# Kernel optimization log

Hardware: AMD Instinct MI355X
Metric: run time of the kernel (lower is better)

The kernel has to match this reference:

```python
import jax, jax.numpy as jnp
import numpy as np
from jax import lax

B, T, H = 128, 8192, 96


def setup_inputs() -> dict:
    key = jax.random.key(0)
    ks = jax.random.split(key, 7)
    s = 1.0 / np.sqrt(H)  # PyTorch LSTM init scale
    return {
        "x": jax.random.normal(ks[0], (B, T, 1), dtype=jnp.float32),
        "w_ih": jax.random.uniform(ks[1], (4 * H, 1), jnp.float32, -s, s),
        "w_hh": jax.random.uniform(ks[2], (4 * H, H), jnp.float32, -s, s),
        "b_ih": jax.random.uniform(ks[3], (4 * H,), jnp.float32, -s, s),
        "b_hh": jax.random.uniform(ks[4], (4 * H,), jnp.float32, -s, s),
        "w_out": jax.random.uniform(ks[5], (1, H), jnp.float32, -s, s),
        "b_out": jax.random.uniform(ks[6], (1,), jnp.float32, -s, s),
    }


def reference(x, w_ih, w_hh, b_ih, b_hh, w_out, b_out):
    # x: [B, T, 1]; single-layer batch_first LSTM, zero initial (h, c).
    Bb, Tt, _ = x.shape
    Hh = w_hh.shape[1]
    # Precompute input contribution to all gates: [T, B, 4H]
    xg = jnp.einsum("bti,gi->btg", x, w_ih) + b_ih + b_hh
    xg = jnp.transpose(xg, (1, 0, 2))

    def step(carry, g):
        h, c = carry
        gates = g + h @ w_hh.T  # [B, 4H]
        i, f, gg, o = jnp.split(gates, 4, axis=-1)  # PyTorch order: i, f, g, o
        i = jax.nn.sigmoid(i)
        f = jax.nn.sigmoid(f)
        gg = jnp.tanh(gg)
        o = jax.nn.sigmoid(o)
        c = f * c + i * gg
        h = o * jnp.tanh(c)
        return (h, c), h

    h0 = jnp.zeros((Bb, Hh), x.dtype)
    (_, _), hs = lax.scan(step, (h0, h0), xg)  # hs: [T, B, H]
    hs = jnp.transpose(hs, (1, 0, 2))  # [B, T, H]
    return hs @ w_out.T + b_out  # [B, T, 1]
```

## Files before the change

kernel.cpp:

```cpp
#include <hip/hip_runtime.h>


#define T_LEN 8192
#define H_DIM 96
#define NTHR  320
#define CHUNK 128
#define LOG2E 1.44269504f

typedef float    f32x4 __attribute__((ext_vector_type(4)));
typedef _Float16 half8 __attribute__((ext_vector_type(8)));

#define MFMA16(A, B, C)                                                        \
    __builtin_amdgcn_mfma_f32_16x16x32_f16(__builtin_bit_cast(half8, (A)),     \
                                           __builtin_bit_cast(half8, (B)),     \
                                           (C), 0, 0, 0)

__device__ __forceinline__ float sig2(float s) {
    return __builtin_amdgcn_rcpf(1.0f + __builtin_amdgcn_exp2f(-s));
}
__device__ __forceinline__ float tanh2(float sg) {
    return 1.0f - 2.0f * __builtin_amdgcn_rcpf(1.0f + __builtin_amdgcn_exp2f(sg));
}

__device__ __forceinline__ f32x4 load_afrag(const float* __restrict__ w_hh,
                                            const float* __restrict__ w_out,
                                            int mt, int kt, int m, int quad) {
    half8 f;
    if (mt < 24) {
        const int r = m & 3;
        const float scale = (r == 2) ? 2.0f * LOG2E : LOG2E;
        const int orig = r * 96 + 4 * mt + (m >> 2);
        const float* src = w_hh + orig * H_DIM + kt * 32 + quad * 8;
        #pragma unroll
        for (int jj = 0; jj < 8; ++jj) f[jj] = (_Float16)(scale * src[jj]);
    } else {
        #pragma unroll
        for (int jj = 0; jj < 8; ++jj)
            f[jj] = (m == 0) ? (_Float16)w_out[kt * 32 + quad * 8 + jj]
                             : (_Float16)0.0f;
    }
    return __builtin_bit_cast(f32x4, f);
}

__global__ __launch_bounds__(NTHR, 2) void lstm_mfma16_kernel(
    const float* __restrict__ x,
    const float* __restrict__ w_ih,
    const float* __restrict__ w_hh,
    const float* __restrict__ b_ih,
    const float* __restrict__ b_hh,
    const float* __restrict__ w_out,
    const float* __restrict__ b_out,
    float* __restrict__ y)
{
    const int tid  = threadIdx.x;
    const int wv   = tid >> 6;
    const int lane = tid & 63;
    const int m    = lane & 15;
    const int quad = lane >> 4;
    const int cc   = m & 7;
    const int bsub = m >> 3;

    __shared__ __align__(16) _Float16 h_s[2][2][H_DIM];
    __shared__ __align__(16) float    y_buf[2][2][CHUNK];
    __shared__ __align__(16) float    x_s[2][T_LEN + 8];

    {
        const float* xpair = x + (size_t)(2 * blockIdx.x) * T_LEN;
        for (int i = tid * 4; i < T_LEN; i += NTHR * 4) {
            *reinterpret_cast<f32x4*>(&x_s[0][i]) =
                *reinterpret_cast<const f32x4*>(&xpair[i]);
            *reinterpret_cast<f32x4*>(&x_s[1][i]) =
                *reinterpret_cast<const f32x4*>(&xpair[T_LEN + i]);
        }
    }

    const int mt0 = 6 * wv;
    f32x4 af00 = load_afrag(w_hh, w_out, mt0 + 0, 0, m, quad);
    f32x4 af01 = load_afrag(w_hh, w_out, mt0 + 0, 1, m, quad);
    f32x4 af02 = load_afrag(w_hh, w_out, mt0 + 0, 2, m, quad);
    f32x4 af10 = load_afrag(w_hh, w_out, mt0 + 1, 0, m, quad);
    f32x4 af11 = load_afrag(w_hh, w_out, mt0 + 1, 1, m, quad);
    f32x4 af12 = load_afrag(w_hh, w_out, mt0 + 1, 2, m, quad);
    f32x4 af20 = load_afrag(w_hh, w_out, mt0 + 2, 0, m, quad);
    f32x4 af21 = load_afrag(w_hh, w_out, mt0 + 2, 1, m, quad);
    f32x4 af22 = load_afrag(w_hh, w_out, mt0 + 2, 2, m, quad);
    f32x4 af30 = load_afrag(w_hh, w_out, mt0 + 3, 0, m, quad);
    f32x4 af31 = load_afrag(w_hh, w_out, mt0 + 3, 1, m, quad);
    f32x4 af32 = load_afrag(w_hh, w_out, mt0 + 3, 2, m, quad);
    f32x4 af40 = load_afrag(w_hh, w_out, mt0 + 4, 0, m, quad);
    f32x4 af41 = load_afrag(w_hh, w_out, mt0 + 4, 1, m, quad);
    f32x4 af42 = load_afrag(w_hh, w_out, mt0 + 4, 2, m, quad);
    f32x4 af50 = load_afrag(w_hh, w_out, mt0 + 5, 0, m, quad);
    f32x4 af51 = load_afrag(w_hh, w_out, mt0 + 5, 1, m, quad);
    f32x4 af52 = load_afrag(w_hh, w_out, mt0 + 5, 2, m, quad);
    f32x4 zero4 = {0.f, 0.f, 0.f, 0.f};
    asm volatile("" : "+v"(af00), "+v"(af01), "+v"(af02), "+v"(af10),
                      "+v"(af11), "+v"(af12), "+v"(af20));
    asm volatile("" : "+v"(af21), "+v"(af22), "+v"(af30), "+v"(af31),
                      "+v"(af32), "+v"(af40), "+v"(af41));
    asm volatile("" : "+v"(af42), "+v"(af50), "+v"(af51), "+v"(af52),
                      "+v"(zero4));

    f32x4 woa0 = {0,0,0,0}, woa1 = {0,0,0,0}, wob0 = {0,0,0,0},
          wob1 = {0,0,0,0}, woc0 = {0,0,0,0}, woc1 = {0,0,0,0};
    if (wv == 4) {
        woa0 = *reinterpret_cast<const f32x4*>(&w_out[quad * 8]);
        woa1 = *reinterpret_cast<const f32x4*>(&w_out[quad * 8 + 4]);
        wob0 = *reinterpret_cast<const f32x4*>(&w_out[32 + quad * 8]);
        wob1 = *reinterpret_cast<const f32x4*>(&w_out[32 + quad * 8 + 4]);
        woc0 = *reinterpret_cast<const f32x4*>(&w_out[64 + quad * 8]);
        woc1 = *reinterpret_cast<const f32x4*>(&w_out[64 + quad * 8 + 4]);
    }

    const int sel  = (cc >= 6) ? (cc - 6) : cc;
    const int cell = (wv < 4) ? (24 * wv + 4 * sel + quad) : 0;
    const bool s_b0 = sel & 1;
    const bool s_b1 = (sel >> 1) & 1;
    const bool s_b2 = (sel >> 2) & 1;
    const float bias_i = LOG2E * (b_ih[0 * H_DIM + cell] + b_hh[0 * H_DIM + cell]);
    const float bias_f = LOG2E * (b_ih[1 * H_DIM + cell] + b_hh[1 * H_DIM + cell]);
    const float bias_g = 2.0f * LOG2E * (b_ih[2 * H_DIM + cell] + b_hh[2 * H_DIM + cell]);
    const float bias_o = LOG2E * (b_ih[3 * H_DIM + cell] + b_hh[3 * H_DIM + cell]);
    const float wih_i  = LOG2E * w_ih[0 * H_DIM + cell];
    const float wih_f  = LOG2E * w_ih[1 * H_DIM + cell];
    const float wih_g  = 2.0f * LOG2E * w_ih[2 * H_DIM + cell];
    const float wih_o  = LOG2E * w_ih[3 * H_DIM + cell];
    const float bout   = b_out[0];
    float c = 0.f;
    if (tid < 2 * H_DIM) (&h_s[0][0][0])[tid] = (_Float16)0.0f;
    __syncthreads();

    if (wv < 4) __builtin_amdgcn_s_setprio(1);

    float x_cur_next = x_s[bsub][0];

    #pragma unroll 2
    for (int it = 0; it <= T_LEN + 1; ++it) {
        const int p = it & 1;

        if (wv < 4) {
            if (it < T_LEN) {
                const f32x4 b0 = *reinterpret_cast<const f32x4*>(&h_s[p][bsub][quad * 8]);
                const f32x4 b1 = *reinterpret_cast<const f32x4*>(&h_s[p][bsub][32 + quad * 8]);
                const f32x4 b2 = *reinterpret_cast<const f32x4*>(&h_s[p][bsub][64 + quad * 8]);
                const float x_cur = x_cur_next;
                x_cur_next = x_s[bsub][it + 1];

                f32x4 acc0 = MFMA16(af00, b0, zero4);
                f32x4 acc1 = MFMA16(af10, b0, zero4);
                f32x4 acc2 = MFMA16(af20, b0, zero4);
                f32x4 acc3 = MFMA16(af30, b0, zero4);
                f32x4 acc4 = MFMA16(af40, b0, zero4);
                f32x4 acc5 = MFMA16(af50, b0, zero4);
                acc0 = MFMA16(af01, b1, acc0);
                acc1 = MFMA16(af11, b1, acc1);
                acc2 = MFMA16(af21, b1, acc2);
                acc3 = MFMA16(af31, b1, acc3);
                acc4 = MFMA16(af41, b1, acc4);
                acc5 = MFMA16(af51, b1, acc5);
                acc0 = MFMA16(af02, b2, acc0);
                acc1 = MFMA16(af12, b2, acc1);
                acc2 = MFMA16(af22, b2, acc2);
                acc3 = MFMA16(af32, b2, acc3);
                acc4 = MFMA16(af42, b2, acc4);
                acc5 = MFMA16(af52, b2, acc5);

                const f32x4 t0 = s_b0 ? acc1 : acc0;
                const f32x4 t1 = s_b0 ? acc3 : acc2;
                const f32x4 t2 = s_b0 ? acc5 : acc4;
                const f32x4 g4 = s_b2 ? t2 : (s_b1 ? t1 : t0);

                const float s0 = g4.x + fmaf(x_cur, wih_i, bias_i);
                const float s1 = g4.y + fmaf(x_cur, wih_f, bias_f);
                const float s2 = g4.z + fmaf(x_cur, wih_g, bias_g);
                const float s3 = g4.w + fmaf(x_cur, wih_o, bias_o);
                const float ig = sig2(s0);
                const float fg = sig2(s1);
                const float gg = tanh2(s2);
                const float og = sig2(s3);
                c = fmaf(fg, c, ig * gg);
                const float h = og * tanh2(2.0f * LOG2E * c);
                h_s[p ^ 1][bsub][cell] = (_Float16)h;
            }
        } else {
            if (it <= T_LEN) {
                const f32x4 b0 = *reinterpret_cast<const f32x4*>(&h_s[p][bsub][quad * 8]);
                const f32x4 b1 = *reinterpret_cast<const f32x4*>(&h_s[p][bsub][32 + quad * 8]);
                const f32x4 b2 = *reinterpret_cast<const f32x4*>(&h_s[p][bsub][64 + quad * 8]);
                const half8 hb0 = __builtin_bit_cast(half8, b0);
                const half8 hb1 = __builtin_bit_cast(half8, b1);
                const half8 hb2 = __builtin_bit_cast(half8, b2);
                float a0 = 0.f, a1 = 0.f, a2 = 0.f;
                a0 = fmaf((float)hb0[0], woa0.x, a0);
                a1 = fmaf((float)hb1[0], wob0.x, a1);
                a2 = fmaf((float)hb2[0], woc0.x, a2);
                a0 = fmaf((float)hb0[1], woa0.y, a0);
                a1 = fmaf((float)hb1[1], wob0.y, a1);
                a2 = fmaf((float)hb2[1], woc0.y, a2);
                a0 = fmaf((float)hb0[2], woa0.z, a0);
                a1 = fmaf((float)hb1[2], wob0.z, a1);
                a2 = fmaf((float)hb2[2], woc0.z, a2);
                a0 = fmaf((float)hb0[3], woa0.w, a0);
                a1 = fmaf((float)hb1[3], wob0.w, a1);
                a2 = fmaf((float)hb2[3], woc0.w, a2);
                a0 = fmaf((float)hb0[4], woa1.x, a0);
                a1 = fmaf((float)hb1[4], wob1.x, a1);
                a2 = fmaf((float)hb2[4], woc1.x, a2);
                a0 = fmaf((float)hb0[5], woa1.y, a0);
                a1 = fmaf((float)hb1[5], wob1.y, a1);
                a2 = fmaf((float)hb2[5], woc1.y, a2);
                a0 = fmaf((float)hb0[6], woa1.z, a0);
                a1 = fmaf((float)hb1[6], wob1.z, a1);
                a2 = fmaf((float)hb2[6], woc1.z, a2);
                a0 = fmaf((float)hb0[7], woa1.w, a0);
                a1 = fmaf((float)hb1[7], wob1.w, a1);
                a2 = fmaf((float)hb2[7], woc1.w, a2);
                float acc = a0 + a1 + a2;
                acc += __shfl_xor(acc, 32, 64);
                acc += __shfl_xor(acc, 16, 64);
                if ((lane == 0 || lane == 8) && it > 0)
                    y_buf[bsub][((it - 1) >> 7) & 1][(it - 1) & (CHUNK - 1)] =
                        acc + bout;
            }
            if ((it & (CHUNK - 1)) == 1 && it > 1) {
                const int base = it - 1 - CHUNK;
                const int pb   = (base >> 7) & 1;
                const int bsel = lane >> 5;
                const int li   = lane & 31;
                const f32x4 v =
                    *reinterpret_cast<const f32x4*>(&y_buf[bsel][pb][li * 4]);
                float* yrow = y + (size_t)(2 * blockIdx.x + bsel) * T_LEN;
                *reinterpret_cast<f32x4*>(&yrow[base + li * 4]) = v;
            }
        }
        __syncthreads();
    }
}

extern "C" void kernel_launch(void* const* d_in, const int* in_sizes, int n_in,
                              void* d_out, int out_size, void* d_ws, size_t ws_size,
                              hipStream_t stream) {
    const float* x     = (const float*)d_in[0];
    const float* w_ih  = (const float*)d_in[1];
    const float* w_hh  = (const float*)d_in[2];
    const float* b_ih  = (const float*)d_in[3];
    const float* b_hh  = (const float*)d_in[4];
    const float* w_out = (const float*)d_in[5];
    const float* b_out = (const float*)d_in[6];
    float* y = (float*)d_out;

    const int NBLK = 64;
    lstm_mfma16_kernel<<<dim3(NBLK), dim3(NTHR), 0, stream>>>(
        x, w_ih, w_hh, b_ih, b_hh, w_out, b_out, y);
}
```

Measured before the change: 3.078 ms.

## Fold output projection into recurrent wave and drop dedicated output wave

```diff
diff --git a/kernel.cpp b/kernel.cpp
--- a/kernel.cpp
+++ b/kernel.cpp
@@ -3,7 +3,7 @@
 
 #define T_LEN 8192
 #define H_DIM 96
-#define NTHR  320
+#define NTHR  256
 #define CHUNK 128
 #define LOG2E 1.44269504f
 
@@ -23,26 +23,18 @@
 }
 
 __device__ __forceinline__ f32x4 load_afrag(const float* __restrict__ w_hh,
-                                            const float* __restrict__ w_out,
                                             int mt, int kt, int m, int quad) {
     half8 f;
-    if (mt < 24) {
-        const int r = m & 3;
-        const float scale = (r == 2) ? 2.0f * LOG2E : LOG2E;
-        const int orig = r * 96 + 4 * mt + (m >> 2);
-        const float* src = w_hh + orig * H_DIM + kt * 32 + quad * 8;
-        #pragma unroll
-        for (int jj = 0; jj < 8; ++jj) f[jj] = (_Float16)(scale * src[jj]);
-    } else {
-        #pragma unroll
-        for (int jj = 0; jj < 8; ++jj)
-            f[jj] = (m == 0) ? (_Float16)w_out[kt * 32 + quad * 8 + jj]
-                             : (_Float16)0.0f;
-    }
+    const int r = m & 3;
+    const float scale = (r == 2) ? 2.0f * LOG2E : LOG2E;
+    const int orig = r * 96 + 4 * mt + (m >> 2);
+    const float* src = w_hh + orig * H_DIM + kt * 32 + quad * 8;
+    #pragma unroll
+    for (int jj = 0; jj < 8; ++jj) f[jj] = (_Float16)(scale * src[jj]);
     return __builtin_bit_cast(f32x4, f);
 }
 
-__global__ __launch_bounds__(NTHR, 2) void lstm_mfma16_kernel(
+__global__ __launch_bounds__(NTHR, 2) void lstm_mfma17_kernel(
     const float* __restrict__ x,
     const float* __restrict__ w_ih,
     const float* __restrict__ w_hh,
@@ -75,24 +67,24 @@
     }
 
     const int mt0 = 6 * wv;
-    f32x4 af00 = load_afrag(w_hh, w_out, mt0 + 0, 0, m, quad);
-    f32x4 af01 = load_afrag(w_hh, w_out, mt0 + 0, 1, m, quad);
-    f32x4 af02 = load_afrag(w_hh, w_out, mt0 + 0, 2, m, quad);
-    f32x4 af10 = load_afrag(w_hh, w_out, mt0 + 1, 0, m, quad);
-    f32x4 af11 = load_afrag(w_hh, w_out, mt0 + 1, 1, m, quad);
-    f32x4 af12 = load_afrag(w_hh, w_out, mt0 + 1, 2, m, quad);
-    f32x4 af20 = load_afrag(w_hh, w_out, mt0 + 2, 0, m, quad);
-    f32x4 af21 = load_afrag(w_hh, w_out, mt0 + 2, 1, m, quad);
-    f32x4 af22 = load_afrag(w_hh, w_out, mt0 + 2, 2, m, quad);
-    f32x4 af30 = load_afrag(w_hh, w_out, mt0 + 3, 0, m, quad);
-    f32x4 af31 = load_afrag(w_hh, w_out, mt0 + 3, 1, m, quad);
-    f32x4 af32 = load_afrag(w_hh, w_out, mt0 + 3, 2, m, quad);
-    f32x4 af40 = load_afrag(w_hh, w_out, mt0 + 4, 0, m, quad);
-    f32x4 af41 = load_afrag(w_hh, w_out, mt0 + 4, 1, m, quad);
-    f32x4 af42 = load_afrag(w_hh, w_out, mt0 + 4, 2, m, quad);
-    f32x4 af50 = load_afrag(w_hh, w_out, mt0 + 5, 0, m, quad);
-    f32x4 af51 = load_afrag(w_hh, w_out, mt0 + 5, 1, m, quad);
-    f32x4 af52 = load_afrag(w_hh, w_out, mt0 + 5, 2, m, quad);
+    f32x4 af00 = load_afrag(w_hh, mt0 + 0, 0, m, quad);
+    f32x4 af01 = load_afrag(w_hh, mt0 + 0, 1, m, quad);
+    f32x4 af02 = load_afrag(w_hh, mt0 + 0, 2, m, quad);
+    f32x4 af10 = load_afrag(w_hh, mt0 + 1, 0, m, quad);
+    f32x4 af11 = load_afrag(w_hh, mt0 + 1, 1, m, quad);
+    f32x4 af12 = load_afrag(w_hh, mt0 + 1, 2, m, quad);
+    f32x4 af20 = load_afrag(w_hh, mt0 + 2, 0, m, quad);
+    f32x4 af21 = load_afrag(w_hh, mt0 + 2, 1, m, quad);
+    f32x4 af22 = load_afrag(w_hh, mt0 + 2, 2, m, quad);
+    f32x4 af30 = load_afrag(w_hh, mt0 + 3, 0, m, quad);
+    f32x4 af31 = load_afrag(w_hh, mt0 + 3, 1, m, quad);
+    f32x4 af32 = load_afrag(w_hh, mt0 + 3, 2, m, quad);
+    f32x4 af40 = load_afrag(w_hh, mt0 + 4, 0, m, quad);
+    f32x4 af41 = load_afrag(w_hh, mt0 + 4, 1, m, quad);
+    f32x4 af42 = load_afrag(w_hh, mt0 + 4, 2, m, quad);
+    f32x4 af50 = load_afrag(w_hh, mt0 + 5, 0, m, quad);
+    f32x4 af51 = load_afrag(w_hh, mt0 + 5, 1, m, quad);
+    f32x4 af52 = load_afrag(w_hh, mt0 + 5, 2, m, quad);
     f32x4 zero4 = {0.f, 0.f, 0.f, 0.f};
     asm volatile("" : "+v"(af00), "+v"(af01), "+v"(af02), "+v"(af10),
                       "+v"(af11), "+v"(af12), "+v"(af20));
@@ -103,7 +95,7 @@
 
     f32x4 woa0 = {0,0,0,0}, woa1 = {0,0,0,0}, wob0 = {0,0,0,0},
           wob1 = {0,0,0,0}, woc0 = {0,0,0,0}, woc1 = {0,0,0,0};
-    if (wv == 4) {
+    if (wv == 0) {
         woa0 = *reinterpret_cast<const f32x4*>(&w_out[quad * 8]);
         woa1 = *reinterpret_cast<const f32x4*>(&w_out[quad * 8 + 4]);
         wob0 = *reinterpret_cast<const f32x4*>(&w_out[32 + quad * 8]);
@@ -111,9 +103,11 @@
         woc0 = *reinterpret_cast<const f32x4*>(&w_out[64 + quad * 8]);
         woc1 = *reinterpret_cast<const f32x4*>(&w_out[64 + quad * 8 + 4]);
     }
+    asm volatile("" : "+v"(woa0), "+v"(woa1), "+v"(wob0), "+v"(wob1),
+                      "+v"(woc0), "+v"(woc1));
 
     const int sel  = (cc >= 6) ? (cc - 6) : cc;
-    const int cell = (wv < 4) ? (24 * wv + 4 * sel + quad) : 0;
+    const int cell = 24 * wv + 4 * sel + quad;
     const bool s_b0 = sel & 1;
     const bool s_b1 = (sel >> 1) & 1;
     const bool s_b2 = (sel >> 2) & 1;
@@ -130,109 +124,108 @@
     if (tid < 2 * H_DIM) (&h_s[0][0][0])[tid] = (_Float16)0.0f;
     __syncthreads();
 
-    if (wv < 4) __builtin_amdgcn_s_setprio(1);
-
     float x_cur_next = x_s[bsub][0];
 
     #pragma unroll 2
     for (int it = 0; it <= T_LEN + 1; ++it) {
         const int p = it & 1;
-
-        if (wv < 4) {
-            if (it < T_LEN) {
-                const f32x4 b0 = *reinterpret_cast<const f32x4*>(&h_s[p][bsub][quad * 8]);
-                const f32x4 b1 = *reinterpret_cast<const f32x4*>(&h_s[p][bsub][32 + quad * 8]);
-                const f32x4 b2 = *reinterpret_cast<const f32x4*>(&h_s[p][bsub][64 + quad * 8]);
-                const float x_cur = x_cur_next;
-                x_cur_next = x_s[bsub][it + 1];
-
-                f32x4 acc0 = MFMA16(af00, b0, zero4);
-                f32x4 acc1 = MFMA16(af10, b0, zero4);
-                f32x4 acc2 = MFMA16(af20, b0, zero4);
-                f32x4 acc3 = MFMA16(af30, b0, zero4);
-                f32x4 acc4 = MFMA16(af40, b0, zero4);
-                f32x4 acc5 = MFMA16(af50, b0, zero4);
-                acc0 = MFMA16(af01, b1, acc0);
-                acc1 = MFMA16(af11, b1, acc1);
-                acc2 = MFMA16(af21, b1, acc2);
-                acc3 = MFMA16(af31, b1, acc3);
-                acc4 = MFMA16(af41, b1, acc4);
-                acc5 = MFMA16(af51, b1, acc5);
-                acc0 = MFMA16(af02, b2, acc0);
-                acc1 = MFMA16(af12, b2, acc1);
-                acc2 = MFMA16(af22, b2, acc2);
-                acc3 = MFMA16(af32, b2, acc3);
-                acc4 = MFMA16(af42, b2, acc4);
-                acc5 = MFMA16(af52, b2, acc5);
-
-                const f32x4 t0 = s_b0 ? acc1 : acc0;
-                const f32x4 t1 = s_b0 ? acc3 : acc2;
-                const f32x4 t2 = s_b0 ? acc5 : acc4;
-                const f32x4 g4 = s_b2 ? t2 : (s_b1 ? t1 : t0);
-
-                const float s0 = g4.x + fmaf(x_cur, wih_i, bias_i);
-                const float s1 = g4.y + fmaf(x_cur, wih_f, bias_f);
-                const float s2 = g4.z + fmaf(x_cur, wih_g, bias_g);
-                const float s3 = g4.w + fmaf(x_cur, wih_o, bias_o);
-                const float ig = sig2(s0);
-                const float fg = sig2(s1);
-                const float gg = tanh2(s2);
-                const float og = sig2(s3);
-                c = fmaf(fg, c, ig * gg);
-                const float h = og * tanh2(2.0f * LOG2E * c);
-                h_s[p ^ 1][bsub][cell] = (_Float16)h;
-            }
-        } else {
-            if (it <= T_LEN) {
-                const f32x4 b0 = *reinterpret_cast<const f32x4*>(&h_s[p][bsub][quad * 8]);
-                const f32x4 b1 = *reinterpret_cast<const f32x4*>(&h_s[p][bsub][32 + quad * 8]);
-                const f32x4 b2 = *reinterpret_cast<const f32x4*>(&h_s[p][bsub][64 + quad * 8]);
-                const half8 hb0 = __builtin_bit_cast(half8, b0);
-                const half8 hb1 = __builtin_bit_cast(half8, b1);
-                const half8 hb2 = __builtin_bit_cast(half8, b2);
-                float a0 = 0.f, a1 = 0.f, a2 = 0.f;
-                a0 = fmaf((float)hb0[0], woa0.x, a0);
-                a1 = fmaf((float)hb1[0], wob0.x, a1);
-                a2 = fmaf((float)hb2[0], woc0.x, a2);
-                a0 = fmaf((float)hb0[1], woa0.y, a0);
-                a1 = fmaf((float)hb1[1], wob0.y, a1);
-                a2 = fmaf((float)hb2[1], woc0.y, a2);
-                a0 = fmaf((float)hb0[2], woa0.z, a0);
-                a1 = fmaf((float)hb1[2], wob0.z, a1);
-                a2 = fmaf((float)hb2[2], woc0.z, a2);
-                a0 = fmaf((float)hb0[3], woa0.w, a0);
-                a1 = fmaf((float)hb1[3], wob0.w, a1);
-                a2 = fmaf((float)hb2[3], woc0.w, a2);
-                a0 = fmaf((float)hb0[4], woa1.x, a0);
-                a1 = fmaf((float)hb1[4], wob1.x, a1);
-                a2 = fmaf((float)hb2[4], woc1.x, a2);
-                a0 = fmaf((float)hb0[5], woa1.y, a0);
-                a1 = fmaf((float)hb1[5], wob1.y, a1);
-                a2 = fmaf((float)hb2[5], woc1.y, a2);
-                a0 = fmaf((float)hb0[6], woa1.z, a0);
-                a1 = fmaf((float)hb1[6], wob1.z, a1);
-                a2 = fmaf((float)hb2[6], woc1.z, a2);
-                a0 = fmaf((float)hb0[7], woa1.w, a0);
-                a1 = fmaf((float)hb1[7], wob1.w, a1);
-                a2 = fmaf((float)hb2[7], woc1.w, a2);
-                float acc = a0 + a1 + a2;
-                acc += __shfl_xor(acc, 32, 64);
-                acc += __shfl_xor(acc, 16, 64);
-                if ((lane == 0 || lane == 8) && it > 0)
-                    y_buf[bsub][((it - 1) >> 7) & 1][(it - 1) & (CHUNK - 1)] =
-                        acc + bout;
-            }
-            if ((it & (CHUNK - 1)) == 1 && it > 1) {
-                const int base = it - 1 - CHUNK;
-                const int pb   = (base >> 7) & 1;
-                const int bsel = lane >> 5;
-                const int li   = lane & 31;
-                const f32x4 v =
-                    *reinterpret_cast<const f32x4*>(&y_buf[bsel][pb][li * 4]);
-                float* yrow = y + (size_t)(2 * blockIdx.x + bsel) * T_LEN;
-                *reinterpret_cast<f32x4*>(&yrow[base + li * 4]) = v;
-            }
-        }
+        const bool rd = (it < T_LEN) || (wv == 0 && it == T_LEN);
+
+        f32x4 b0, b1, b2;
+        const float x_cur = x_cur_next;
+        if (rd) {
+            b0 = *reinterpret_cast<const f32x4*>(&h_s[p][bsub][quad * 8]);
+            b1 = *reinterpret_cast<const f32x4*>(&h_s[p][bsub][32 + quad * 8]);
+            b2 = *reinterpret_cast<const f32x4*>(&h_s[p][bsub][64 + quad * 8]);
+            x_cur_next = x_s[bsub][it + 1];
+        }
+
+        if (it < T_LEN) {
+            f32x4 acc0 = MFMA16(af00, b0, zero4);
+            f32x4 acc1 = MFMA16(af10, b0, zero4);
+            f32x4 acc2 = MFMA16(af20, b0, zero4);
+            f32x4 acc3 = MFMA16(af30, b0, zero4);
+            f32x4 acc4 = MFMA16(af40, b0, zero4);
+            f32x4 acc5 = MFMA16(af50, b0, zero4);
+            acc0 = MFMA16(af01, b1, acc0);
+            acc1 = MFMA16(af11, b1, acc1);
+            acc2 = MFMA16(af21, b1, acc2);
+            acc3 = MFMA16(af31, b1, acc3);
+            acc4 = MFMA16(af41, b1, acc4);
+            acc5 = MFMA16(af51, b1, acc5);
+            acc0 = MFMA16(af02, b2, acc0);
+            acc1 = MFMA16(af12, b2, acc1);
+            acc2 = MFMA16(af22, b2, acc2);
+            acc3 = MFMA16(af32, b2, acc3);
+            acc4 = MFMA16(af42, b2, acc4);
+            acc5 = MFMA16(af52, b2, acc5);
+
+            const f32x4 t0 = s_b0 ? acc1 : acc0;
+            const f32x4 t1 = s_b0 ? acc3 : acc2;
+            const f32x4 t2 = s_b0 ? acc5 : acc4;
+            const f32x4 g4 = s_b2 ? t2 : (s_b1 ? t1 : t0);
+
+            const float s0 = g4.x + fmaf(x_cur, wih_i, bias_i);
+            const float s1 = g4.y + fmaf(x_cur, wih_f, bias_f);
+            const float s2 = g4.z + fmaf(x_cur, wih_g, bias_g);
+            const float s3 = g4.w + fmaf(x_cur, wih_o, bias_o);
+            const float ig = sig2(s0);
+            const float fg = sig2(s1);
+            const float gg = tanh2(s2);
+            const float og = sig2(s3);
+            c = fmaf(fg, c, ig * gg);
+            const float h = og * tanh2(2.0f * LOG2E * c);
+            h_s[p ^ 1][bsub][cell] = (_Float16)h;
+        }
+
+        if (wv == 0 && rd && it > 0) {
+            const half8 hb0 = __builtin_bit_cast(half8, b0);
+            const half8 hb1 = __builtin_bit_cast(half8, b1);
+            const half8 hb2 = __builtin_bit_cast(half8, b2);
+            float a0 = 0.f, a1 = 0.f, a2 = 0.f;
+            a0 = fmaf((float)hb0[0], woa0.x, a0);
+            a1 = fmaf((float)hb1[0], wob0.x, a1);
+            a2 = fmaf((float)hb2[0], woc0.x, a2);
+            a0 = fmaf((float)hb0[1], woa0.y, a0);
+            a1 = fmaf((float)hb1[1], wob0.y, a1);
+            a2 = fmaf((float)hb2[1], woc0.y, a2);
+            a0 = fmaf((float)hb0[2], woa0.z, a0);
+            a1 = fmaf((float)hb1[2], wob0.z, a1);
+            a2 = fmaf((float)hb2[2], woc0.z, a2);
+            a0 = fmaf((float)hb0[3], woa0.w, a0);
+            a1 = fmaf((float)hb1[3], wob0.w, a1);
+            a2 = fmaf((float)hb2[3], woc0.w, a2);
+            a0 = fmaf((float)hb0[4], woa1.x, a0);
+            a1 = fmaf((float)hb1[4], wob1.x, a1);
+            a2 = fmaf((float)hb2[4], woc1.x, a2);
+            a0 = fmaf((float)hb0[5], woa1.y, a0);
+            a1 = fmaf((float)hb1[5], wob1.y, a1);
+            a2 = fmaf((float)hb2[5], woc1.y, a2);
+            a0 = fmaf((float)hb0[6], woa1.z, a0);
+            a1 = fmaf((float)hb1[6], wob1.z, a1);
+            a2 = fmaf((float)hb2[6], woc1.z, a2);
+            a0 = fmaf((float)hb0[7], woa1.w, a0);
+            a1 = fmaf((float)hb1[7], wob1.w, a1);
+            a2 = fmaf((float)hb2[7], woc1.w, a2);
+            float acc = a0 + a1 + a2;
+            acc += __shfl_xor(acc, 32, 64);
+            acc += __shfl_xor(acc, 16, 64);
+            if (lane == 0 || lane == 8)
+                y_buf[bsub][((it - 1) >> 7) & 1][(it - 1) & (CHUNK - 1)] =
+                    acc + bout;
+        }
+
+        if (wv == 1 && (it & (CHUNK - 1)) == 1 && it > 1) {
+            const int base = it - 1 - CHUNK;
+            const int pb   = (base >> 7) & 1;
+            const int bsel = lane >> 5;
+            const int li   = lane & 31;
+            const f32x4 v =
+                *reinterpret_cast<const f32x4*>(&y_buf[bsel][pb][li * 4]);
+            float* yrow = y + (size_t)(2 * blockIdx.x + bsel) * T_LEN;
+            *reinterpret_cast<f32x4*>(&yrow[base + li * 4]) = v;
+        }
+
         __syncthreads();
     }
 }
@@ -250,6 +243,6 @@
     float* y = (float*)d_out;
 
     const int NBLK = 64;
-    lstm_mfma16_kernel<<<dim3(NBLK), dim3(NTHR), 0, stream>>>(
+    lstm_mfma17_kernel<<<dim3(NBLK), dim3(NTHR), 0, stream>>>(
         x, w_ih, w_hh, b_ih, b_hh, w_out, b_out, y);
 }
```

Result: slower. 3.817 ms (+24.0%).
